# Kernel tuning notes

Measured on AMD Instinct MI355X. Metric: run time of the kernel, lower is better.

The kernel has to match this reference:

```python
import jax, jax.numpy as jnp
import numpy as np

SELECTED_CLASSES = 5  # selected_classes init arg; loop body is identical each iteration
EPS = 1e-5            # nn.InstanceNorm2d default eps


def setup_inputs() -> dict:
    key = jax.random.key(0)
    k1, k2, k3 = jax.random.split(key, 3)
    x = jax.random.normal(k1, (8, 256, 128, 128), dtype=jnp.float32)
    masks = jax.random.uniform(k2, (8, 512, 512), dtype=jnp.float32)
    conv_w = jax.random.normal(k3, (1, 3, 7, 7), dtype=jnp.float32) * 0.05  # CFR_branches[0], no bias
    in_gamma = jnp.ones((256,), dtype=jnp.float32)   # InstanceNorm2d affine weight
    in_beta = jnp.zeros((256,), dtype=jnp.float32)   # InstanceNorm2d affine bias
    return {"x": x, "masks": masks, "conv_w": conv_w, "in_gamma": in_gamma, "in_beta": in_beta}


def reference(x, masks, conv_w, in_gamma, in_beta):
    B, C, H, W = x.shape
    m = masks[:, None, :, :] if masks.ndim == 3 else masks  # [B,1,Hm,Wm]
    # F.interpolate(..., size=(H,H), mode='bilinear', align_corners=False) -> half-pixel bilinear
    m = jax.image.resize(m, (B, 1, H, H), method="bilinear")
    mid = x * m                                             # [B,C,H,W]
    avg_out = jnp.mean(mid, axis=1, keepdims=True)          # [B,1,H,W]
    max_out = jnp.max(mid, axis=1, keepdims=True)           # [B,1,H,W]
    atten = jnp.concatenate([avg_out, max_out, m], axis=1)  # [B,3,H,W]
    atten = jax.lax.conv_general_dilated(
        atten, conv_w, window_strides=(1, 1), padding=[(3, 3), (3, 3)],
        dimension_numbers=("NCHW", "OIHW", "NCHW"))        # [B,1,H,W]
    atten = jax.nn.sigmoid(atten)
    out = mid * atten
    # set_class_mask_matrix: kmeans1d is not imported -> except branch -> all-ones mask;
    # Regional_Normalization therefore reduces to InstanceNorm2d(out).
    mu = jnp.mean(out, axis=(2, 3), keepdims=True)
    var = jnp.var(out, axis=(2, 3), keepdims=True)
    rn = (out - mu) * jax.lax.rsqrt(var + EPS)
    rn = rn * in_gamma[None, :, None, None] + in_beta[None, :, None, None]
    # loop over selected_classes produces identical outs (idx stays 0); sum == scale
    return jax.nn.relu(SELECTED_CLASSES * rn)
```

## Files before the change

### kernel.cpp

```cpp
#include <hip/hip_runtime.h>
#include <math.h>

#define BB 8
#define CC 256
#define HH 128
#define WW 128
#define HWP 16384
#define MH 512
#define MW 512
#define NPIX (BB*HWP)
#define IQ 4096

__global__ __launch_bounds__(256) void k1(const float* __restrict__ masks,
                                          const float* __restrict__ x,
                                          float* __restrict__ m_out,
                                          float* __restrict__ cs,
                                          float* __restrict__ cm) {
    int bid = blockIdx.x, tid = threadIdx.x;
    if ((bid & 1) == 0) {
        int t = (bid >> 1) * 256 + tid;
        int j = t & 127, i = (t >> 7) & 127, b = t >> 14;
        const float Wt[8] = {1.f, 3.f, 5.f, 7.f, 7.f, 5.f, 3.f, 1.f};
        const float* mb = masks + (size_t)b * (MH * MW);
        int r0 = 4 * i - 2, c0 = 4 * j - 2;
        float cwgt[8];
        int ccl[8];
        float sh = 0.f;
        #pragma unroll
        for (int q = 0; q < 8; q++) {
            int c = c0 + q;
            bool v = (unsigned)c < (unsigned)MW;
            cwgt[q] = v ? Wt[q] : 0.f;
            sh += cwgt[q];
            ccl[q] = min(max(c, 0), MW - 1);
        }
        float acc = 0.f, sv = 0.f;
        #pragma unroll
        for (int p = 0; p < 8; p++) {
            int r = r0 + p;
            bool v = (unsigned)r < (unsigned)MH;
            float wp = v ? Wt[p] : 0.f;
            sv += wp;
            const float* row = mb + (size_t)min(max(r, 0), MH - 1) * MW;
            float ra = 0.f;
            #pragma unroll
            for (int q = 0; q < 8; q++) ra += cwgt[q] * row[ccl[q]];
            acc += wp * ra;
        }
        m_out[t] = acc / (sv * sh);
    } else {
        int id = bid >> 1;
        int chunk = id & 15;
        int g = (id >> 4) & 3;
        int b = id >> 6;
        int qi = chunk * 256 + tid;
        const float4* xb = (const float4*)x + ((size_t)(b * CC + g * 64)) * IQ + qi;
        float4 s = {0.f, 0.f, 0.f, 0.f};
        float4 mx = {-INFINITY, -INFINITY, -INFINITY, -INFINITY};
        #pragma unroll 8
        for (int c = 0; c < 64; c++) {
            float4 v = xb[(size_t)c * IQ];
            s.x += v.x; s.y += v.y; s.z += v.z; s.w += v.w;
            mx.x = fmaxf(mx.x, v.x); mx.y = fmaxf(mx.y, v.y);
            mx.z = fmaxf(mx.z, v.z); mx.w = fmaxf(mx.w, v.w);
        }
        size_t o = (size_t)g * (NPIX / 4) + (size_t)b * IQ + qi;
        ((float4*)cs)[o] = s;
        ((float4*)cm)[o] = mx;
    }
}

#define TW 64
#define TH 4
#define IW 70
#define IH 10
#define PITCH 72
__global__ __launch_bounds__(256) void k2(const float* __restrict__ m,
                                          const float* __restrict__ cs,
                                          const float* __restrict__ cm,
                                          const float* __restrict__ cw,
                                          float* __restrict__ wprod) {
    __shared__ float w[147];
    __shared__ float pa[IH * PITCH], px[IH * PITCH], pm[IH * PITCH];
    int tid = threadIdx.x, bid = blockIdx.x;
    int bx = bid & 1, by = (bid >> 1) & 31, b = bid >> 6;
    if (tid < 147) w[tid] = cw[tid];
    int ox = bx * TW - 3, oy = by * TH - 3;
    for (int idx = tid; idx < IW * IH; idx += 256) {
        int r = idx / IW, c = idx - r * IW;
        int gi = oy + r, gj = ox + c;
        float av = 0.f, mxv = 0.f, mv = 0.f;
        if ((unsigned)gi < (unsigned)HH && (unsigned)gj < (unsigned)WW) {
            int p = b * HWP + gi * WW + gj;
            mv = m[p];
            float s = cs[p] + cs[p + NPIX] + cs[p + 2 * NPIX] + cs[p + 3 * NPIX];
            float mmx = fmaxf(fmaxf(cm[p], cm[p + NPIX]),
                              fmaxf(cm[p + 2 * NPIX], cm[p + 3 * NPIX]));
            av = mv * s * (1.f / 256.f);
            mxv = mv * mmx;
        }
        pa[r * PITCH + c] = av;
        px[r * PITCH + c] = mxv;
        pm[r * PITCH + c] = mv;
    }
    __syncthreads();
    int col = tid & 63, r = tid >> 6;
    float acc = 0.f;
    #pragma unroll
    for (int di = 0; di < 7; di++) {
        #pragma unroll
        for (int dj = 0; dj < 7; dj++) {
            int li = (r + di) * PITCH + col + dj;
            acc += w[di * 7 + dj] * pa[li];
            acc += w[49 + di * 7 + dj] * px[li];
            acc += w[98 + di * 7 + dj] * pm[li];
        }
    }
    float at = 1.f / (1.f + expf(-acc));
    float res = pm[(r + 3) * PITCH + col + 3] * at;
    wprod[b * HWP + (by * TH + r) * WW + bx * TW + col] = res;
}

__global__ __launch_bounds__(256) void k3(const float* __restrict__ x,
                                          const float* __restrict__ wprod,
                                          const float* __restrict__ gamma,
                                          const float* __restrict__ beta,
                                          float* __restrict__ out) {
    int bc = blockIdx.x;
    int b = bc >> 8, c = bc & 255;
    const float4* xp = (const float4*)(x + (size_t)bc * HWP);
    const float4* wp = (const float4*)(wprod + (size_t)b * HWP);
    float4 o[16];
    float s = 0.f, ss = 0.f;
    #pragma unroll
    for (int k = 0; k < 16; k++) {
        int idx = threadIdx.x + k * 256;
        float4 xv = xp[idx];
        float4 wv = wp[idx];
        float4 ov;
        ov.x = xv.x * wv.x; ov.y = xv.y * wv.y;
        ov.z = xv.z * wv.z; ov.w = xv.w * wv.w;
        o[k] = ov;
        s += ov.x + ov.y + ov.z + ov.w;
        ss += ov.x * ov.x + ov.y * ov.y + ov.z * ov.z + ov.w * ov.w;
    }
    #pragma unroll
    for (int off = 32; off; off >>= 1) {
        s += __shfl_down(s, off, 64);
        ss += __shfl_down(ss, off, 64);
    }
    __shared__ float ls[4], lss[4];
    __shared__ float smu, srs;
    int wave = threadIdx.x >> 6, lane = threadIdx.x & 63;
    if (lane == 0) { ls[wave] = s; lss[wave] = ss; }
    __syncthreads();
    if (threadIdx.x == 0) {
        float S = ls[0] + ls[1] + ls[2] + ls[3];
        float SS = lss[0] + lss[1] + lss[2] + lss[3];
        float mu = S * (1.f / HWP);
        float var = fmaxf(SS * (1.f / HWP) - mu * mu, 0.f);
        smu = mu;
        srs = rsqrtf(var + 1e-5f);
    }
    __syncthreads();
    float mu = smu;
    float g5 = 5.f * srs * gamma[c];
    float b5 = 5.f * beta[c];
    float4* op = (float4*)(out + (size_t)bc * HWP);
    #pragma unroll
    for (int k = 0; k < 16; k++) {
        int idx = threadIdx.x + k * 256;
        float4 ov = o[k], r;
        r.x = fmaxf(fmaf(ov.x - mu, g5, b5), 0.f);
        r.y = fmaxf(fmaf(ov.y - mu, g5, b5), 0.f);
        r.z = fmaxf(fmaf(ov.z - mu, g5, b5), 0.f);
        r.w = fmaxf(fmaf(ov.w - mu, g5, b5), 0.f);
        op[idx] = r;
    }
}

extern "C" void kernel_launch(void* const* d_in, const int* in_sizes, int n_in,
                              void* d_out, int out_size, void* d_ws, size_t ws_size,
                              hipStream_t stream) {
    const float* x      = (const float*)d_in[0];
    const float* masks  = (const float*)d_in[1];
    const float* conv_w = (const float*)d_in[2];
    const float* gamma  = (const float*)d_in[3];
    const float* beta   = (const float*)d_in[4];
    float* out = (float*)d_out;

    float* ws = (float*)d_ws;
    float* m_arr = ws;
    float* cs    = ws + (size_t)NPIX;
    float* cm    = ws + (size_t)5 * NPIX;
    float* wprod = ws + (size_t)9 * NPIX;

    k1<<<1024, 256, 0, stream>>>(masks, x, m_arr, cs, cm);
    k2<<<512, 256, 0, stream>>>(m_arr, cs, cm, conv_w, wprod);
    k3<<<BB * CC, 256, 0, stream>>>(x, wprod, gamma, beta, out);
}
```

Before: 265.0 us.

## Fuse three kernels into one cooperative kernel with grid syncs

Merges the mask-resize/channel-reduction, attention conv, and instance-norm stages into a single cooperative kernel separated by grid-wide barriers, falling back to the three-kernel path if the cooperative launch fails. The aim is to remove two kernel launch gaps and tail effects, and to improve L2 reuse of x between stages. Output stores are also made nontemporal. In exchange the grid is capped at 1024 blocks, so the norm stage loops twice per block, and the grid barriers add their own cost.

```diff
diff --git a/kernel.cpp b/kernel.cpp
--- a/kernel.cpp
+++ b/kernel.cpp
@@ -1,5 +1,8 @@
 #include <hip/hip_runtime.h>
+#include <hip/hip_cooperative_groups.h>
 #include <math.h>
+
+namespace cg = cooperative_groups;
 
 #define BB 8
 #define CC 256
@@ -11,12 +14,28 @@
 #define NPIX (BB*HWP)
 #define IQ 4096
 
-__global__ __launch_bounds__(256) void k1(const float* __restrict__ masks,
-                                          const float* __restrict__ x,
-                                          float* __restrict__ m_out,
-                                          float* __restrict__ cs,
-                                          float* __restrict__ cm) {
-    int bid = blockIdx.x, tid = threadIdx.x;
+#define TW 64
+#define TH 4
+#define IW 70
+#define IH 10
+#define PITCH 72
+
+typedef float f32x4_t __attribute__((ext_vector_type(4)));
+
+__global__ __launch_bounds__(256, 4) void fused(
+    const float* __restrict__ masks, const float* __restrict__ x,
+    const float* __restrict__ cw, const float* __restrict__ gamma,
+    const float* __restrict__ beta, float* __restrict__ out,
+    float* __restrict__ m_out, float* __restrict__ cs,
+    float* __restrict__ cm, float* __restrict__ wprod)
+{
+    cg::grid_group grid = cg::this_grid();
+    __shared__ float w[147];
+    __shared__ float pa[IH * PITCH], px[IH * PITCH], pm[IH * PITCH];
+    __shared__ float ls[4], lss[4], sstat[2];
+
+    const int bid = blockIdx.x, tid = threadIdx.x;
+
     if ((bid & 1) == 0) {
         int t = (bid >> 1) * 256 + tid;
         int j = t & 127, i = (t >> 7) & 127, b = t >> 14;
@@ -68,13 +87,164 @@
         ((float4*)cs)[o] = s;
         ((float4*)cm)[o] = mx;
     }
-}
-
-#define TW 64
-#define TH 4
-#define IW 70
-#define IH 10
-#define PITCH 72
+
+    __threadfence();
+    grid.sync();
+
+    if (bid < 512) {
+        int bx = bid & 1, by = (bid >> 1) & 31, b = bid >> 6;
+        if (tid < 147) w[tid] = cw[tid];
+        int ox = bx * TW - 3, oy = by * TH - 3;
+        for (int idx = tid; idx < IW * IH; idx += 256) {
+            int r = idx / IW, c = idx - r * IW;
+            int gi = oy + r, gj = ox + c;
+            float av = 0.f, mxv = 0.f, mv = 0.f;
+            if ((unsigned)gi < (unsigned)HH && (unsigned)gj < (unsigned)WW) {
+                int p = b * HWP + gi * WW + gj;
+                mv = m_out[p];
+                float sfull = cs[p] + cs[p + NPIX] + cs[p + 2 * NPIX] + cs[p + 3 * NPIX];
+                float mmx = fmaxf(fmaxf(cm[p], cm[p + NPIX]),
+                                  fmaxf(cm[p + 2 * NPIX], cm[p + 3 * NPIX]));
+                av = mv * sfull * (1.f / 256.f);
+                mxv = mv * mmx;
+            }
+            pa[r * PITCH + c] = av;
+            px[r * PITCH + c] = mxv;
+            pm[r * PITCH + c] = mv;
+        }
+        __syncthreads();
+        int col = tid & 63, r = tid >> 6;
+        float acc = 0.f;
+        #pragma unroll
+        for (int di = 0; di < 7; di++) {
+            #pragma unroll
+            for (int dj = 0; dj < 7; dj++) {
+                int li = (r + di) * PITCH + col + dj;
+                acc += w[di * 7 + dj] * pa[li];
+                acc += w[49 + di * 7 + dj] * px[li];
+                acc += w[98 + di * 7 + dj] * pm[li];
+            }
+        }
+        float at = 1.f / (1.f + expf(-acc));
+        float res = pm[(r + 3) * PITCH + col + 3] * at;
+        wprod[b * HWP + (by * TH + r) * WW + bx * TW + col] = res;
+    }
+
+    __threadfence();
+    grid.sync();
+
+    for (int bc = bid; bc < BB * CC; bc += 1024) {
+        int b = bc >> 8, c = bc & 255;
+        const float4* xp = (const float4*)(x + (size_t)bc * HWP);
+        const float4* wpv = (const float4*)(wprod + (size_t)b * HWP);
+        float4 o[16];
+        float s = 0.f, ss = 0.f;
+        #pragma unroll
+        for (int k = 0; k < 16; k++) {
+            int idx = tid + k * 256;
+            float4 xv = xp[idx];
+            float4 wv = wpv[idx];
+            float4 ov;
+            ov.x = xv.x * wv.x; ov.y = xv.y * wv.y;
+            ov.z = xv.z * wv.z; ov.w = xv.w * wv.w;
+            o[k] = ov;
+            s += ov.x + ov.y + ov.z + ov.w;
+            ss += ov.x * ov.x + ov.y * ov.y + ov.z * ov.z + ov.w * ov.w;
+        }
+        #pragma unroll
+        for (int off = 32; off; off >>= 1) {
+            s += __shfl_down(s, off, 64);
+            ss += __shfl_down(ss, off, 64);
+        }
+        int wave = tid >> 6, lane = tid & 63;
+        if (lane == 0) { ls[wave] = s; lss[wave] = ss; }
+        __syncthreads();
+        if (tid == 0) {
+            float S = ls[0] + ls[1] + ls[2] + ls[3];
+            float SS = lss[0] + lss[1] + lss[2] + lss[3];
+            float mu = S * (1.f / HWP);
+            float var = fmaxf(SS * (1.f / HWP) - mu * mu, 0.f);
+            sstat[0] = mu;
+            sstat[1] = rsqrtf(var + 1e-5f);
+        }
+        __syncthreads();
+        float mu = sstat[0];
+        float g5 = 5.f * sstat[1] * gamma[c];
+        float b5 = 5.f * beta[c];
+        float* op = out + (size_t)bc * HWP;
+        #pragma unroll
+        for (int k = 0; k < 16; k++) {
+            int idx = tid + k * 256;
+            float4 ov = o[k];
+            f32x4_t r;
+            r.x = fmaxf(fmaf(ov.x - mu, g5, b5), 0.f);
+            r.y = fmaxf(fmaf(ov.y - mu, g5, b5), 0.f);
+            r.z = fmaxf(fmaf(ov.z - mu, g5, b5), 0.f);
+            r.w = fmaxf(fmaf(ov.w - mu, g5, b5), 0.f);
+            __builtin_nontemporal_store(r, ((f32x4_t*)op) + idx);
+        }
+    }
+}
+
+__global__ __launch_bounds__(256) void k1(const float* __restrict__ masks,
+                                          const float* __restrict__ x,
+                                          float* __restrict__ m_out,
+                                          float* __restrict__ cs,
+                                          float* __restrict__ cm) {
+    int bid = blockIdx.x, tid = threadIdx.x;
+    if ((bid & 1) == 0) {
+        int t = (bid >> 1) * 256 + tid;
+        int j = t & 127, i = (t >> 7) & 127, b = t >> 14;
+        const float Wt[8] = {1.f, 3.f, 5.f, 7.f, 7.f, 5.f, 3.f, 1.f};
+        const float* mb = masks + (size_t)b * (MH * MW);
+        int r0 = 4 * i - 2, c0 = 4 * j - 2;
+        float cwgt[8];
+        int ccl[8];
+        float sh = 0.f;
+        #pragma unroll
+        for (int q = 0; q < 8; q++) {
+            int c = c0 + q;
+            bool v = (unsigned)c < (unsigned)MW;
+            cwgt[q] = v ? Wt[q] : 0.f;
+            sh += cwgt[q];
+            ccl[q] = min(max(c, 0), MW - 1);
+        }
+        float acc = 0.f, sv = 0.f;
+        #pragma unroll
+        for (int p = 0; p < 8; p++) {
+            int r = r0 + p;
+            bool v = (unsigned)r < (unsigned)MH;
+            float wp = v ? Wt[p] : 0.f;
+            sv += wp;
+            const float* row = mb + (size_t)min(max(r, 0), MH - 1) * MW;
+            float ra = 0.f;
+            #pragma unroll
+            for (int q = 0; q < 8; q++) ra += cwgt[q] * row[ccl[q]];
+            acc += wp * ra;
+        }
+        m_out[t] = acc / (sv * sh);
+    } else {
+        int id = bid >> 1;
+        int chunk = id & 15;
+        int g = (id >> 4) & 3;
+        int b = id >> 6;
+        int qi = chunk * 256 + tid;
+        const float4* xb = (const float4*)x + ((size_t)(b * CC + g * 64)) * IQ + qi;
+        float4 s = {0.f, 0.f, 0.f, 0.f};
+        float4 mx = {-INFINITY, -INFINITY, -INFINITY, -INFINITY};
+        #pragma unroll 8
+        for (int c = 0; c < 64; c++) {
+            float4 v = xb[(size_t)c * IQ];
+            s.x += v.x; s.y += v.y; s.z += v.z; s.w += v.w;
+            mx.x = fmaxf(mx.x, v.x); mx.y = fmaxf(mx.y, v.y);
+            mx.z = fmaxf(mx.z, v.z); mx.w = fmaxf(mx.w, v.w);
+        }
+        size_t o = (size_t)g * (NPIX / 4) + (size_t)b * IQ + qi;
+        ((float4*)cs)[o] = s;
+        ((float4*)cm)[o] = mx;
+    }
+}
+
 __global__ __launch_bounds__(256) void k2(const float* __restrict__ m,
                                           const float* __restrict__ cs,
                                           const float* __restrict__ cm,
@@ -187,7 +357,7 @@
     const float* conv_w = (const float*)d_in[2];
     const float* gamma  = (const float*)d_in[3];
     const float* beta   = (const float*)d_in[4];
-    float* out = (float*)d_out;
+    float* outp = (float*)d_out;
 
     float* ws = (float*)d_ws;
     float* m_arr = ws;
@@ -195,7 +365,14 @@
     float* cm    = ws + (size_t)5 * NPIX;
     float* wprod = ws + (size_t)9 * NPIX;
 
-    k1<<<1024, 256, 0, stream>>>(masks, x, m_arr, cs, cm);
-    k2<<<512, 256, 0, stream>>>(m_arr, cs, cm, conv_w, wprod);
-    k3<<<BB * CC, 256, 0, stream>>>(x, wprod, gamma, beta, out);
-}
+    void* args[] = {(void*)&masks, (void*)&x, (void*)&conv_w, (void*)&gamma,
+                    (void*)&beta, (void*)&outp, (void*)&m_arr, (void*)&cs,
+                    (void*)&cm, (void*)&wprod};
+    hipError_t err = hipLaunchCooperativeKernel((const void*)fused, dim3(1024),
+                                                dim3(256), args, 0, stream);
+    if (err != hipSuccess) {
+        k1<<<1024, 256, 0, stream>>>(masks, x, m_arr, cs, cm);
+        k2<<<512, 256, 0, stream>>>(m_arr, cs, cm, conv_w, wprod);
+        k3<<<BB * CC, 256, 0, stream>>>(x, wprod, gamma, beta, outp);
+    }
+}
```

New measurement: 717.0 us. 2.71x slower.
